# Kernel optimization log

Measured on AMD Instinct MI355X. Metric: run time of the kernel, lower is better.

The kernel has to match this reference:

```python
import jax, jax.numpy as jnp
import numpy as np

N = 100000   # nodes
E = 1600000  # edges
G = 256      # graphs in batch
IN = 128     # in_feats
H = 64       # h_feats


def _xavier(k, shape):
    fan_in, fan_out = shape
    lim = float(np.sqrt(6.0 / (fan_in + fan_out)))
    return jax.random.uniform(k, shape, jnp.float32, -lim, lim)


def setup_inputs() -> dict:
    key = jax.random.key(0)
    ks = jax.random.split(key, 12)
    x = jax.random.normal(ks[0], (N, IN), jnp.float32)
    src = jax.random.randint(ks[1], (E,), 0, N)
    dst = jax.random.randint(ks[2], (E,), 0, N)
    ew = jax.random.uniform(ks[3], (E,), jnp.float32)
    gid = jnp.sort(jax.random.randint(ks[4], (N,), 0, G))
    def lin(k, fi, fo):
        kw, kb = jax.random.split(k)
        lim = float(np.sqrt(1.0 / fi))
        return (jax.random.uniform(kw, (fi, fo), jnp.float32, -lim, lim),
                jax.random.uniform(kb, (fo,), jnp.float32, -lim, lim))
    W1 = _xavier(ks[5], (IN, H)); b1 = jnp.zeros((H,), jnp.float32)
    W2 = _xavier(ks[6], (H, H));  b2 = jnp.zeros((H,), jnp.float32)
    W3 = _xavier(ks[7], (H, H));  b3 = jnp.zeros((H,), jnp.float32)
    Dw1, Db1 = lin(ks[8], H, 16)
    Dw2, Db2 = lin(ks[9], 16, 8)
    Dw3, Db3 = lin(ks[10], 8, 1)
    return {"x": x, "src": src, "dst": dst, "ew": ew, "gid": gid,
            "W1": W1, "b1": b1, "W2": W2, "b2": b2, "W3": W3, "b3": b3,
            "Dw1": Dw1, "Db1": Db1, "Dw2": Dw2, "Db2": Db2, "Dw3": Dw3, "Db3": Db3}


def reference(x, src, dst, ew, gid, W1, b1, W2, b2, W3, b3,
              Dw1, Db1, Dw2, Db2, Dw3, Db3):
    n = x.shape[0]
    # DGL GraphConv norm='both': unweighted degrees, clamped to >= 1
    deg_out = jnp.zeros((n,), x.dtype).at[src].add(1.0)
    deg_in = jnp.zeros((n,), x.dtype).at[dst].add(1.0)
    ns = jax.lax.rsqrt(jnp.maximum(deg_out, 1.0))  # src-side norm
    nd = jax.lax.rsqrt(jnp.maximum(deg_in, 1.0))   # dst-side norm

    def conv(h, W, b):
        # apply weight first (in >= out), then gather-scale-scatter
        h = (h * ns[:, None]) @ W                      # [N, out]
        m = h[src] * ew[:, None]                       # [E, out] edge messages
        agg = jnp.zeros((n, W.shape[1]), h.dtype).at[dst].add(m)
        return agg * nd[:, None] + b

    h = jax.nn.relu(conv(x, W1, b1))
    h = jax.nn.relu(conv(h, W2, b2))
    h = jax.nn.relu(conv(h, W3, b3))

    # mean_nodes: per-graph mean pooling
    counts = jnp.zeros((G,), h.dtype).at[gid].add(1.0)
    pooled = jnp.zeros((G, h.shape[1]), h.dtype).at[gid].add(h)
    pooled = pooled / jnp.maximum(counts, 1.0)[:, None]

    h = jax.nn.relu(pooled @ Dw1 + Db1)
    h = jax.nn.relu(h @ Dw2 + Db2)
    return jax.nn.sigmoid(h @ Dw3 + Db3)  # [G, 1]
```

## Files before the change

kernel.cpp:

```cpp
#include <hip/hip_runtime.h>
#include <math.h>

#define N_NODES 100000
#define N_EDGES 1600000
#define G_GRAPHS 256
#define IN_F 128
#define H_F 64

#define HB 20
#define HCHUNK (N_EDGES / HB)
#define NWORDS (N_NODES / 4)
#define HNODES 25000
#define HWORDS (HNODES / 4)
#define HR 4

#define NREG 160
#define REG_NODES 625
#define BUCKET_CAP 11000
#define BSPAN 6400
#define NB_BUCKET (N_EDGES / BSPAN)

#define NTILES_C 6250
#define NB_GEMMW 391

typedef unsigned int uint_t;
typedef unsigned short ushort_t;
typedef unsigned char uchar_t;
typedef __attribute__((ext_vector_type(8))) short short8;
typedef __attribute__((ext_vector_type(4))) float floatx4;
typedef __attribute__((ext_vector_type(2))) float floatx2;

__device__ __forceinline__ ushort_t f2bf(float f) {
  uint_t u = __float_as_uint(f);
  uint_t r = (u + 0x7fffu + ((u >> 16) & 1u)) >> 16;
  return (ushort_t)r;
}
__device__ __forceinline__ float bflo(uint_t u) { return __uint_as_float(u << 16); }
__device__ __forceinline__ uchar_t f2fp8(float f) {
  return (uchar_t)(__builtin_amdgcn_cvt_pk_fp8_f32(f, f, 0, false) & 0xff);
}
__device__ __forceinline__ int sw_idx(int row, int kshort) {
  int slot = kshort >> 3;
  return row * 64 + (((slot ^ (row & 7)) << 3) | (kshort & 7));
}

__global__ __launch_bounds__(256) void build_a_kernel(
    const int* __restrict__ src, const int* __restrict__ dst,
    const float* __restrict__ ew, int* __restrict__ bcnt,
    uint2* __restrict__ bucket, uint_t* __restrict__ p8src) {
  __shared__ uint_t shm[BSPAN + 2 * NREG];
  if (blockIdx.x < NB_BUCKET) {
    uint_t* rl = shm;
    int* cnt = (int*)(shm + BSPAN);
    int* cur = cnt + NREG;
    const int e0 = blockIdx.x * BSPAN;

    for (int i = threadIdx.x; i < NREG; i += 256) cnt[i] = 0;
    __syncthreads();

    for (int i = threadIdx.x; i < BSPAN; i += 256) {
      uint_t d = (uint_t)dst[e0 + i];
      uint_t r = d / REG_NODES;
      uint_t loc = d - r * REG_NODES;
      rl[i] = (r << 16) | loc;
      atomicAdd(&cnt[r], 1);
    }
    __syncthreads();

    for (int i = threadIdx.x; i < NREG; i += 256)
      cur[i] = atomicAdd(&bcnt[i], cnt[i]);
    __syncthreads();

    for (int i = threadIdx.x; i < BSPAN; i += 256) {
      uint_t v = rl[i];
      uint_t r = v >> 16, loc = v & 0xffffu;
      int pos = atomicAdd(&cur[r], 1);
      if (pos < BUCKET_CAP)
        bucket[(size_t)r * BUCKET_CAP + pos] = make_uint2(
            (loc << 17) | (uint_t)src[e0 + i], __float_as_uint(ew[e0 + i]));
    }
  } else {
    uint_t* h = shm;
    const int idx = blockIdx.x - NB_BUCKET;
    const int r = idx / HB;
    const int b = idx % HB;
    const uint_t rbase = (uint_t)(r * HNODES);

    for (int i = threadIdx.x; i < HWORDS; i += 256) h[i] = 0u;
    __syncthreads();

    const uint4* k4 = (const uint4*)(src + b * HCHUNK);
    for (int i = threadIdx.x; i < HCHUNK / 4; i += 256) {
      uint4 v = k4[i];
      uint_t t;
      t = v.x - rbase; if (t < (uint_t)HNODES) atomicAdd(&h[t >> 2], 1u << ((t & 3u) * 8u));
      t = v.y - rbase; if (t < (uint_t)HNODES) atomicAdd(&h[t >> 2], 1u << ((t & 3u) * 8u));
      t = v.z - rbase; if (t < (uint_t)HNODES) atomicAdd(&h[t >> 2], 1u << ((t & 3u) * 8u));
      t = v.w - rbase; if (t < (uint_t)HNODES) atomicAdd(&h[t >> 2], 1u << ((t & 3u) * 8u));
    }
    __syncthreads();

    uint_t* outp = p8src + (size_t)b * NWORDS + r * HWORDS;
    for (int i = threadIdx.x; i < HWORDS; i += 256) outp[i] = h[i];
  }
}

__global__ __launch_bounds__(1024, 2) void buildb_gemm_kernel(
    const uint2* __restrict__ bucket, const int* __restrict__ bcnt,
    const uint_t* __restrict__ p8src, const float* __restrict__ x,
    const float* __restrict__ W1, uint_t* __restrict__ csr,
    int2* __restrict__ rc, float* __restrict__ nd, float* __restrict__ ns,
    uchar_t* __restrict__ T) {
  __shared__ __align__(16) char shm_u[53104];
  const int tid = threadIdx.x;

  if (blockIdx.x >= NREG) {
    constexpr int WROW = IN_F + 8;
    ushort_t* Wt = (ushort_t*)shm_u;
    float* ns_s = (float*)(shm_u + 17408);

    for (int i = tid; i < IN_F * 64; i += 1024) {
      int k = i >> 6, nn = i & 63;
      Wt[nn * WROW + k] = f2bf(W1[i]);
    }
    __syncthreads();

    const int wv = tid >> 6;
    const int lane = tid & 63;
    const int tile = (blockIdx.x - NREG) * 16 + wv;
    if (tile >= NTILES_C) return;
    const int node0 = tile * 16;
    const int m = lane & 15;
    const int q = lane >> 4;

    if (lane < 4) {
      const int w = tile * 4 + lane;
      int c0 = 0, c1 = 0, c2 = 0, c3 = 0;
      for (int b = 0; b < HB; ++b) {
        uint_t xv = p8src[(size_t)b * NWORDS + w];
        c0 += (int)(xv & 0xffu);
        c1 += (int)((xv >> 8) & 0xffu);
        c2 += (int)((xv >> 16) & 0xffu);
        c3 += (int)((xv >> 24) & 0xffu);
      }
      float4 nv = make_float4(
          rsqrtf(fmaxf((float)c0, 1.0f)), rsqrtf(fmaxf((float)c1, 1.0f)),
          rsqrtf(fmaxf((float)c2, 1.0f)), rsqrtf(fmaxf((float)c3, 1.0f)));
      ((float4*)ns)[w] = nv;
      *(float4*)&ns_s[wv * 16 + lane * 4] = nv;
    }

    short8 afrag[4];
    const float* xr = x + (size_t)(node0 + m) * IN_F + q * 8;
#pragma unroll
    for (int c = 0; c < 4; ++c) {
      float4 xa = *(const float4*)(xr + c * 32);
      float4 xb = *(const float4*)(xr + c * 32 + 4);
      short8 a;
      a[0] = (short)f2bf(xa.x); a[1] = (short)f2bf(xa.y);
      a[2] = (short)f2bf(xa.z); a[3] = (short)f2bf(xa.w);
      a[4] = (short)f2bf(xb.x); a[5] = (short)f2bf(xb.y);
      a[6] = (short)f2bf(xb.z); a[7] = (short)f2bf(xb.w);
      afrag[c] = a;
    }

    floatx4 acc[4];
#pragma unroll
    for (int t = 0; t < 4; ++t) acc[t] = (floatx4){0.f, 0.f, 0.f, 0.f};
#pragma unroll
    for (int t = 0; t < 4; ++t) {
      const ushort_t* wr = &Wt[(t * 16 + m) * WROW + q * 8];
#pragma unroll
      for (int c = 0; c < 4; ++c) {
        short8 bfrag = *(const short8*)(wr + c * 32);
        acc[t] = __builtin_amdgcn_mfma_f32_16x16x32_bf16(afrag[c], bfrag,
                                                         acc[t], 0, 0, 0);
      }
    }
#pragma unroll
    for (int t = 0; t < 4; ++t) {
#pragma unroll
      for (int r = 0; r < 4; ++r) {
        int node = node0 + q * 4 + r;
        T[(size_t)node * 64 + t * 16 + m] =
            f2fp8(acc[t][r] * ns_s[wv * 16 + q * 4 + r]);
      }
    }
    return;
  }

  uint_t* staged = (uint_t*)shm_u;
  int* cnt = (int*)(shm_u + 44000);
  int* sc = (int*)(shm_u + 46500);
  int* ts = (int*)(shm_u + 49000);
  const int r = blockIdx.x;
  const int nE = min(bcnt[r], BUCKET_CAP);

  ts[tid] = (tid < NREG) ? min(bcnt[tid], BUCKET_CAP) : 0;
  for (int i = tid; i < REG_NODES; i += 1024) cnt[i] = 0;
  __syncthreads();
  for (int off = 1; off < 256; off <<= 1) {
    int t = (tid >= off) ? ts[tid - off] : 0;
    __syncthreads();
    ts[tid] += t;
    __syncthreads();
  }
  const int csr_base = (r == 0) ? 0 : ts[r - 1];
  __syncthreads();

  const uint2* bk = bucket + (size_t)r * BUCKET_CAP;
  for (int i = tid; i < nE; i += 1024) atomicAdd(&cnt[bk[i].x >> 17], 1);
  __syncthreads();

  int cv = (tid < REG_NODES) ? cnt[tid] : 0;
  ts[tid] = cv;
  __syncthreads();
  for (int off = 1; off < 1024; off <<= 1) {
    int t = (tid >= off) ? ts[tid - off] : 0;
    __syncthreads();
    ts[tid] += t;
    __syncthreads();
  }
  if (tid < REG_NODES) {
    int run = (tid == 0) ? 0 : ts[tid - 1];
    sc[tid] = run;
    int v = r * REG_NODES + tid;
    rc[v] = make_int2(csr_base + run, cv);
    nd[v] = rsqrtf(fmaxf((float)cv, 1.0f));
  }
  __syncthreads();

  for (int i = tid; i < nE; i += 1024) {
    uint2 e = bk[i];
    uint_t loc = e.x >> 17;
    int pos = atomicAdd(&sc[loc], 1);
    staged[pos] = ((uint_t)(f2bf(__uint_as_float(e.y)) & 0x7fff) << 17) |
                  (e.x & 0x1ffffu);
  }
  __syncthreads();

  for (int i = tid; i < nE; i += 1024) csr[csr_base + i] = staged[i];
}

__device__ __forceinline__ void gacc1(float acc[8], uint_t e, uint2 p) {
  float w = __uint_as_float((e >> 17) << 16);
  floatx2 a;
  a = __builtin_amdgcn_cvt_pk_f32_fp8(p.x, false);
  acc[0] = fmaf(a.x, w, acc[0]); acc[1] = fmaf(a.y, w, acc[1]);
  a = __builtin_amdgcn_cvt_pk_f32_fp8(p.x, true);
  acc[2] = fmaf(a.x, w, acc[2]); acc[3] = fmaf(a.y, w, acc[3]);
  a = __builtin_amdgcn_cvt_pk_f32_fp8(p.y, false);
  acc[4] = fmaf(a.x, w, acc[4]); acc[5] = fmaf(a.y, w, acc[5]);
  a = __builtin_amdgcn_cvt_pk_f32_fp8(p.y, true);
  acc[6] = fmaf(a.x, w, acc[6]); acc[7] = fmaf(a.y, w, acc[7]);
}

template <bool POOL>
__global__ __launch_bounds__(256, 6) void fused_kernel(
    const uint_t* __restrict__ csr, const int2* __restrict__ rc,
    const uchar_t* __restrict__ T, const float* __restrict__ nd,
    const float* __restrict__ bias, const float* __restrict__ ns,
    const float* __restrict__ W, uchar_t* __restrict__ Tout,
    const int* __restrict__ gid, float* __restrict__ pooled) {
  __shared__ __align__(16) ushort_t Hs[POOL ? 8 : 64 * 64];
  __shared__ __align__(16) ushort_t Wt[POOL ? 8 : 64 * 64];
  __shared__ float gaccF[POOL ? 256 : 1];
  __shared__ int g0s;
  const int tid = threadIdx.x;
  const int node_base = blockIdx.x * 64;
  const int vlast = min(node_base + 63, N_NODES - 1);

  if constexpr (POOL) {
    gaccF[tid] = 0.0f;
    if (tid == 0) g0s = gid[node_base];
  } else {
    for (int i = tid; i < H_F * 64; i += 256) {
      int k = i >> 6, nn = i & 63;
      Wt[sw_idx(nn, k)] = f2bf(W[i]);
    }
  }
  __syncthreads();

  const int lane = tid & 63;
  const int wv = tid >> 6;
  const int o = lane >> 3, l = lane & 7;
  const uint2* Tp = (const uint2*)T;

  const float4 b0 = *(const float4*)&bias[l * 8];
  const float4 b1v = *(const float4*)&bias[l * 8 + 4];

#pragma unroll 1
  for (int pass = 0; pass < 2; ++pass) {
    const int ln = pass * 32 + wv * 8 + o;
    const int v = node_base + ln;
    if (v < N_NODES) {
      int2 rcv = rc[v];
      int k = rcv.x;
      const int ke = rcv.x + rcv.y;
      float acc[8] = {0, 0, 0, 0, 0, 0, 0, 0};

      for (; k + 4 <= ke; k += 4) {
        uint_t e0 = csr[k], e1 = csr[k + 1], e2 = csr[k + 2], e3 = csr[k + 3];
        uint2 p0 = Tp[(size_t)(e0 & 0x1ffffu) * 8 + l];
        uint2 p1 = Tp[(size_t)(e1 & 0x1ffffu) * 8 + l];
        uint2 p2 = Tp[(size_t)(e2 & 0x1ffffu) * 8 + l];
        uint2 p3 = Tp[(size_t)(e3 & 0x1ffffu) * 8 + l];
        gacc1(acc, e0, p0); gacc1(acc, e1, p1);
        gacc1(acc, e2, p2); gacc1(acc, e3, p3);
      }
      for (; k < ke; ++k) {
        uint_t e0 = csr[k];
        uint2 p0 = Tp[(size_t)(e0 & 0x1ffffu) * 8 + l];
        gacc1(acc, e0, p0);
      }

      const float ndv = nd[v];
      if constexpr (!POOL) {
        uint4 ov;
        ov.x = (uint_t)f2bf(fmaxf(fmaf(acc[0], ndv, b0.x), 0.f)) |
               ((uint_t)f2bf(fmaxf(fmaf(acc[1], ndv, b0.y), 0.f)) << 16);
        ov.y = (uint_t)f2bf(fmaxf(fmaf(acc[2], ndv, b0.z), 0.f)) |
               ((uint_t)f2bf(fmaxf(fmaf(acc[3], ndv, b0.w), 0.f)) << 16);
        ov.z = (uint_t)f2bf(fmaxf(fmaf(acc[4], ndv, b1v.x), 0.f)) |
               ((uint_t)f2bf(fmaxf(fmaf(acc[5], ndv, b1v.y), 0.f)) << 16);
        ov.w = (uint_t)f2bf(fmaxf(fmaf(acc[6], ndv, b1v.z), 0.f)) |
               ((uint_t)f2bf(fmaxf(fmaf(acc[7], ndv, b1v.w), 0.f)) << 16);
        *((uint4*)&Hs[sw_idx(ln, l * 8)]) = ov;
      } else {
        const float bb[8] = {b0.x, b0.y, b0.z, b0.w, b1v.x, b1v.y, b1v.z, b1v.w};
        float vals[8];
#pragma unroll
        for (int f = 0; f < 8; ++f)
          vals[f] = bflo((uint_t)f2bf(fmaxf(fmaf(acc[f], ndv, bb[f]), 0.f)));
        int g = gid[v];
        int gl = g - g0s;
        if (gl >= 0 && gl < 4) {
#pragma unroll
          for (int f = 0; f < 8; ++f)
            atomicAdd(&gaccF[gl * 64 + l * 8 + f], vals[f]);
        } else {
#pragma unroll
          for (int f = 0; f < 8; ++f)
            atomicAdd(&pooled[(size_t)g * 64 + l * 8 + f], vals[f]);
        }
      }
    }
  }
  __syncthreads();

  if constexpr (!POOL) {
    const int m = lane & 15, q = lane >> 4;
    const int node0 = node_base + wv * 16;
    if (node0 < N_NODES) {
      short8 afrag[2];
      afrag[0] = *(const short8*)&Hs[sw_idx(wv * 16 + m, q * 8)];
      afrag[1] = *(const short8*)&Hs[sw_idx(wv * 16 + m, q * 8 + 32)];

      floatx4 acc4v[4];
#pragma unroll
      for (int t = 0; t < 4; ++t) acc4v[t] = (floatx4){0.f, 0.f, 0.f, 0.f};
#pragma unroll
      for (int t = 0; t < 4; ++t) {
#pragma unroll
        for (int c = 0; c < 2; ++c) {
          short8 bfrag = *(const short8*)&Wt[sw_idx(t * 16 + m, q * 8 + c * 32)];
          acc4v[t] = __builtin_amdgcn_mfma_f32_16x16x32_bf16(afrag[c], bfrag,
                                                            acc4v[t], 0, 0, 0);
        }
      }
      float4 nsv = *(const float4*)(ns + node0 + q * 4);
      const float nsa[4] = {nsv.x, nsv.y, nsv.z, nsv.w};
#pragma unroll
      for (int t = 0; t < 4; ++t) {
#pragma unroll
        for (int r2 = 0; r2 < 4; ++r2) {
          int node = node0 + q * 4 + r2;
          Tout[(size_t)node * 64 + t * 16 + m] = f2fp8(acc4v[t][r2] * nsa[r2]);
        }
      }
    }
  } else {
    int span = gid[vlast] - g0s + 1;
    if (span > 4) span = 4;
    if (tid < span * 64) {
      int gl = tid >> 6, j = tid & 63;
      int g = g0s + gl;
      if (g < G_GRAPHS) {
        float vsum = gaccF[gl * 64 + j];
        if (vsum != 0.0f) atomicAdd(&pooled[(size_t)g * 64 + j], vsum);
      }
    }
  }
}

__global__ __launch_bounds__(256) void pool_mlp_kernel(
    const float* __restrict__ pooled, const int* __restrict__ gid,
    const float* __restrict__ Dw1, const float* __restrict__ Db1,
    const float* __restrict__ Dw2, const float* __restrict__ Db2,
    const float* __restrict__ Dw3, const float* __restrict__ Db3,
    float* __restrict__ out) {
  __shared__ float mean[64];
  __shared__ float h1s[16], h2s[8];
  const int g = blockIdx.x;
  int l = 0, r = N_NODES;
  while (l < r) { int m = (l + r) >> 1; if (gid[m] < g) l = m + 1; else r = m; }
  const int lo = l;
  r = N_NODES;
  while (l < r) { int m = (l + r) >> 1; if (gid[m] < g + 1) l = m + 1; else r = m; }
  const int hi = l;

  if (threadIdx.x < 64) {
    float inv = 1.0f / fmaxf((float)(hi - lo), 1.0f);
    mean[threadIdx.x] = pooled[(size_t)g * 64 + threadIdx.x] * inv;
  }
  __syncthreads();
  if (threadIdx.x < 16) {
    int o = threadIdx.x;
    float a = Db1[o];
#pragma unroll
    for (int k = 0; k < 64; ++k) a = fmaf(mean[k], Dw1[k * 16 + o], a);
    h1s[o] = fmaxf(a, 0.0f);
  }
  __syncthreads();
  if (threadIdx.x < 8) {
    int o = threadIdx.x;
    float a = Db2[o];
#pragma unroll
    for (int k = 0; k < 16; ++k) a = fmaf(h1s[k], Dw2[k * 8 + o], a);
    h2s[o] = fmaxf(a, 0.0f);
  }
  __syncthreads();
  if (threadIdx.x == 0) {
    float a = Db3[0];
#pragma unroll
    for (int k = 0; k < 8; ++k) a = fmaf(h2s[k], Dw3[k], a);
    out[g] = 1.0f / (1.0f + expf(-a));
  }
}

extern "C" void kernel_launch(void* const* d_in, const int* in_sizes, int n_in,
                              void* d_out, int out_size, void* d_ws, size_t ws_size,
                              hipStream_t stream) {
  const float* x   = (const float*)d_in[0];
  const int*   src = (const int*)  d_in[1];
  const int*   dst = (const int*)  d_in[2];
  const float* ew  = (const float*)d_in[3];
  const int*   gid = (const int*)  d_in[4];
  const float* W1  = (const float*)d_in[5];
  const float* b1  = (const float*)d_in[6];
  const float* W2  = (const float*)d_in[7];
  const float* b2  = (const float*)d_in[8];
  const float* W3  = (const float*)d_in[9];
  const float* b3  = (const float*)d_in[10];
  const float* Dw1 = (const float*)d_in[11];
  const float* Db1 = (const float*)d_in[12];
  const float* Dw2 = (const float*)d_in[13];
  const float* Db2 = (const float*)d_in[14];
  const float* Dw3 = (const float*)d_in[15];
  const float* Db3 = (const float*)d_in[16];
  float* out = (float*)d_out;

  char* p = (char*)d_ws;
  uint2*    bucket = (uint2*)p;          p += (size_t)NREG * BUCKET_CAP * 8;
  uint_t*   csr   = (uint_t*)p;          p += (size_t)N_EDGES * 4;
  uint_t*   p8src = (uint_t*)p;          p += (size_t)HB * NWORDS * 4;
  float*    ns    = (float*)p;           p += (size_t)N_NODES * 4;
  float*    nd    = (float*)p;           p += (size_t)N_NODES * 4;
  int2*     rc    = (int2*)p;            p += (size_t)N_NODES * 8;
  int*      bcnt  = (int*)p;             p += (size_t)NREG * 4;
  float*    pooled = (float*)p;          p += (size_t)G_GRAPHS * H_F * 4;
  uchar_t*  T_a   = (uchar_t*)p;         p += (size_t)N_NODES * 64;
  uchar_t*  T_b   = (uchar_t*)p;

  const int NB_A = NB_BUCKET + HR * HB;
  const int NB_M = NREG + NB_GEMMW;
  const int NB_F = (N_NODES + 63) / 64;

  hipMemsetAsync(bcnt, 0,
                 NREG * sizeof(int) + G_GRAPHS * H_F * sizeof(float), stream);
  build_a_kernel<<<NB_A, 256, 0, stream>>>(src, dst, ew, bcnt, bucket, p8src);
  buildb_gemm_kernel<<<NB_M, 1024, 0, stream>>>(bucket, bcnt, p8src, x, W1,
                                                csr, rc, nd, ns, T_a);
  fused_kernel<false><<<NB_F, 256, 0, stream>>>(csr, rc, T_a, nd, b1, ns, W2,
                                                T_b, nullptr, nullptr);
  fused_kernel<false><<<NB_F, 256, 0, stream>>>(csr, rc, T_b, nd, b2, ns, W3,
                                                T_a, nullptr, nullptr);
  fused_kernel<true><<<NB_F, 256, 0, stream>>>(csr, rc, T_a, nd, b3, nullptr,
                                               nullptr, nullptr, gid, pooled);
  pool_mlp_kernel<<<G_GRAPHS, 256, 0, stream>>>(pooled, gid, Dw1, Db1, Dw2, Db2,
                                                Dw3, Db3, out);
}
```

Baseline: 306.8 us.

## Split CSR by source half and gather in two grid-synced phases

The CSR build now partitions each destination's edges by whether the source node falls in the lower or upper half of node ids, and stores the split count in the high bits of rc. The fused layer kernels become cooperative launches with 128 nodes per block and 4 nodes per lane-group held in registers. Every block first gathers from low-half sources, hits a grid-wide sync, then gathers from high-half sources. This keeps the set of fp8 feature rows being read at any one time small enough to stay resident in cache. It adds grid-sync cost, lowers occupancy (launch bounds 4) and replaces the swizzled LDS layout with padded rows.

```diff
diff --git a/kernel.cpp b/kernel.cpp
--- a/kernel.cpp
+++ b/kernel.cpp
@@ -1,5 +1,8 @@
 #include <hip/hip_runtime.h>
+#include <hip/hip_cooperative_groups.h>
 #include <math.h>
+
+namespace cg = cooperative_groups;
 
 #define N_NODES 100000
 #define N_EDGES 1600000
@@ -22,6 +25,8 @@
 
 #define NTILES_C 6250
 #define NB_GEMMW 391
+#define SRC_HALF 50000
+#define NB_F2 782
 
 typedef unsigned int uint_t;
 typedef unsigned short ushort_t;
@@ -30,6 +35,8 @@
 typedef __attribute__((ext_vector_type(4))) float floatx4;
 typedef __attribute__((ext_vector_type(2))) float floatx2;
 
+constexpr int WROW_F = H_F + 8;
+
 __device__ __forceinline__ ushort_t f2bf(float f) {
   uint_t u = __float_as_uint(f);
   uint_t r = (u + 0x7fffu + ((u >> 16) & 1u)) >> 16;
@@ -38,10 +45,6 @@
 __device__ __forceinline__ float bflo(uint_t u) { return __uint_as_float(u << 16); }
 __device__ __forceinline__ uchar_t f2fp8(float f) {
   return (uchar_t)(__builtin_amdgcn_cvt_pk_fp8_f32(f, f, 0, false) & 0xff);
-}
-__device__ __forceinline__ int sw_idx(int row, int kshort) {
-  int slot = kshort >> 3;
-  return row * 64 + (((slot ^ (row & 7)) << 3) | (kshort & 7));
 }
 
 __global__ __launch_bounds__(256) void build_a_kernel(
@@ -111,7 +114,7 @@
     const float* __restrict__ W1, uint_t* __restrict__ csr,
     int2* __restrict__ rc, float* __restrict__ nd, float* __restrict__ ns,
     uchar_t* __restrict__ T) {
-  __shared__ __align__(16) char shm_u[53104];
+  __shared__ __align__(16) char shm_u[58112];
   const int tid = threadIdx.x;
 
   if (blockIdx.x >= NREG) {
@@ -190,14 +193,14 @@
   }
 
   uint_t* staged = (uint_t*)shm_u;
-  int* cnt = (int*)(shm_u + 44000);
-  int* sc = (int*)(shm_u + 46500);
-  int* ts = (int*)(shm_u + 49000);
+  int* cnt2 = (int*)(shm_u + 44000);
+  int* sc2 = (int*)(shm_u + 49000);
+  int* ts = (int*)(shm_u + 54000);
   const int r = blockIdx.x;
   const int nE = min(bcnt[r], BUCKET_CAP);
 
   ts[tid] = (tid < NREG) ? min(bcnt[tid], BUCKET_CAP) : 0;
-  for (int i = tid; i < REG_NODES; i += 1024) cnt[i] = 0;
+  for (int i = tid; i < REG_NODES * 2; i += 1024) cnt2[i] = 0;
   __syncthreads();
   for (int off = 1; off < 256; off <<= 1) {
     int t = (tid >= off) ? ts[tid - off] : 0;
@@ -209,10 +212,19 @@
   __syncthreads();
 
   const uint2* bk = bucket + (size_t)r * BUCKET_CAP;
-  for (int i = tid; i < nE; i += 1024) atomicAdd(&cnt[bk[i].x >> 17], 1);
-  __syncthreads();
-
-  int cv = (tid < REG_NODES) ? cnt[tid] : 0;
+  for (int i = tid; i < nE; i += 1024) {
+    uint_t ex = bk[i].x;
+    uint_t loc = ex >> 17;
+    uint_t q = ((ex & 0x1ffffu) >= SRC_HALF) ? 1u : 0u;
+    atomicAdd(&cnt2[loc * 2 + q], 1);
+  }
+  __syncthreads();
+
+  int c0 = 0, cv = 0;
+  if (tid < REG_NODES) {
+    c0 = cnt2[tid * 2];
+    cv = c0 + cnt2[tid * 2 + 1];
+  }
   ts[tid] = cv;
   __syncthreads();
   for (int off = 1; off < 1024; off <<= 1) {
@@ -223,9 +235,10 @@
   }
   if (tid < REG_NODES) {
     int run = (tid == 0) ? 0 : ts[tid - 1];
-    sc[tid] = run;
+    sc2[tid * 2] = run;
+    sc2[tid * 2 + 1] = run + c0;
     int v = r * REG_NODES + tid;
-    rc[v] = make_int2(csr_base + run, cv);
+    rc[v] = make_int2(csr_base + run, cv | (c0 << 16));
     nd[v] = rsqrtf(fmaxf((float)cv, 1.0f));
   }
   __syncthreads();
@@ -233,7 +246,8 @@
   for (int i = tid; i < nE; i += 1024) {
     uint2 e = bk[i];
     uint_t loc = e.x >> 17;
-    int pos = atomicAdd(&sc[loc], 1);
+    uint_t q = ((e.x & 0x1ffffu) >= SRC_HALF) ? 1u : 0u;
+    int pos = atomicAdd(&sc2[loc * 2 + q], 1);
     staged[pos] = ((uint_t)(f2bf(__uint_as_float(e.y)) & 0x7fff) << 17) |
                   (e.x & 0x1ffffu);
   }
@@ -255,20 +269,55 @@
   acc[6] = fmaf(a.x, w, acc[6]); acc[7] = fmaf(a.y, w, acc[7]);
 }
 
+__device__ __forceinline__ void gather_seg(const uint_t* __restrict__ csr,
+                                           const uint2* __restrict__ Tp, int l,
+                                           int s, int e, float acc[8]) {
+  int k = s;
+  while (k + 8 <= e) {
+    uint_t eb[8];
+    uint2 pb[8];
+#pragma unroll
+    for (int j = 0; j < 8; ++j) eb[j] = csr[k + j];
+#pragma unroll
+    for (int j = 0; j < 8; ++j)
+      pb[j] = Tp[(size_t)(eb[j] & 0x1ffffu) * 8 + l];
+#pragma unroll
+    for (int j = 0; j < 8; ++j) gacc1(acc, eb[j], pb[j]);
+    k += 8;
+  }
+  if (k + 4 <= e) {
+    uint_t eb[4];
+    uint2 pb[4];
+#pragma unroll
+    for (int j = 0; j < 4; ++j) eb[j] = csr[k + j];
+#pragma unroll
+    for (int j = 0; j < 4; ++j)
+      pb[j] = Tp[(size_t)(eb[j] & 0x1ffffu) * 8 + l];
+#pragma unroll
+    for (int j = 0; j < 4; ++j) gacc1(acc, eb[j], pb[j]);
+    k += 4;
+  }
+  for (; k < e; ++k) {
+    uint_t e0 = csr[k];
+    uint2 p0 = Tp[(size_t)(e0 & 0x1ffffu) * 8 + l];
+    gacc1(acc, e0, p0);
+  }
+}
+
 template <bool POOL>
-__global__ __launch_bounds__(256, 6) void fused_kernel(
+__global__ __launch_bounds__(256, 4) void fused_kernel(
     const uint_t* __restrict__ csr, const int2* __restrict__ rc,
     const uchar_t* __restrict__ T, const float* __restrict__ nd,
     const float* __restrict__ bias, const float* __restrict__ ns,
     const float* __restrict__ W, uchar_t* __restrict__ Tout,
     const int* __restrict__ gid, float* __restrict__ pooled) {
-  __shared__ __align__(16) ushort_t Hs[POOL ? 8 : 64 * 64];
-  __shared__ __align__(16) ushort_t Wt[POOL ? 8 : 64 * 64];
+  __shared__ __align__(16) ushort_t Hs[POOL ? 8 : 128 * WROW_F];
+  __shared__ __align__(16) ushort_t Wt[POOL ? 8 : 64 * WROW_F];
   __shared__ float gaccF[POOL ? 256 : 1];
   __shared__ int g0s;
   const int tid = threadIdx.x;
-  const int node_base = blockIdx.x * 64;
-  const int vlast = min(node_base + 63, N_NODES - 1);
+  const int node_base = blockIdx.x * 128;
+  const int vlast = min(node_base + 127, N_NODES - 1);
 
   if constexpr (POOL) {
     gaccF[tid] = 0.0f;
@@ -276,7 +325,7 @@
   } else {
     for (int i = tid; i < H_F * 64; i += 256) {
       int k = i >> 6, nn = i & 63;
-      Wt[sw_idx(nn, k)] = f2bf(W[i]);
+      Wt[nn * WROW_F + k] = f2bf(W[i]);
     }
   }
   __syncthreads();
@@ -289,49 +338,60 @@
   const float4 b0 = *(const float4*)&bias[l * 8];
   const float4 b1v = *(const float4*)&bias[l * 8 + 4];
 
-#pragma unroll 1
-  for (int pass = 0; pass < 2; ++pass) {
-    const int ln = pass * 32 + wv * 8 + o;
+  int2 rcv[4];
+#pragma unroll
+  for (int p = 0; p < 4; ++p) {
+    const int v = node_base + p * 32 + wv * 8 + o;
+    rcv[p] = (v < N_NODES) ? rc[v] : make_int2(0, 0);
+  }
+
+  float acc[4][8];
+#pragma unroll
+  for (int p = 0; p < 4; ++p)
+#pragma unroll
+    for (int f = 0; f < 8; ++f) acc[p][f] = 0.0f;
+
+#pragma unroll
+  for (int p = 0; p < 4; ++p) {
+    const int s = rcv[p].x;
+    const int h0 = ((uint_t)rcv[p].y) >> 16;
+    gather_seg(csr, Tp, l, s, s + h0, acc[p]);
+  }
+
+  cg::this_grid().sync();
+
+#pragma unroll
+  for (int p = 0; p < 4; ++p) {
+    const int s = rcv[p].x;
+    const int h0 = ((uint_t)rcv[p].y) >> 16;
+    const int cnt = rcv[p].y & 0xffff;
+    gather_seg(csr, Tp, l, s + h0, s + cnt, acc[p]);
+  }
+
+#pragma unroll
+  for (int p = 0; p < 4; ++p) {
+    const int ln = p * 32 + wv * 8 + o;
     const int v = node_base + ln;
     if (v < N_NODES) {
-      int2 rcv = rc[v];
-      int k = rcv.x;
-      const int ke = rcv.x + rcv.y;
-      float acc[8] = {0, 0, 0, 0, 0, 0, 0, 0};
-
-      for (; k + 4 <= ke; k += 4) {
-        uint_t e0 = csr[k], e1 = csr[k + 1], e2 = csr[k + 2], e3 = csr[k + 3];
-        uint2 p0 = Tp[(size_t)(e0 & 0x1ffffu) * 8 + l];
-        uint2 p1 = Tp[(size_t)(e1 & 0x1ffffu) * 8 + l];
-        uint2 p2 = Tp[(size_t)(e2 & 0x1ffffu) * 8 + l];
-        uint2 p3 = Tp[(size_t)(e3 & 0x1ffffu) * 8 + l];
-        gacc1(acc, e0, p0); gacc1(acc, e1, p1);
-        gacc1(acc, e2, p2); gacc1(acc, e3, p3);
-      }
-      for (; k < ke; ++k) {
-        uint_t e0 = csr[k];
-        uint2 p0 = Tp[(size_t)(e0 & 0x1ffffu) * 8 + l];
-        gacc1(acc, e0, p0);
-      }
-
       const float ndv = nd[v];
       if constexpr (!POOL) {
         uint4 ov;
-        ov.x = (uint_t)f2bf(fmaxf(fmaf(acc[0], ndv, b0.x), 0.f)) |
-               ((uint_t)f2bf(fmaxf(fmaf(acc[1], ndv, b0.y), 0.f)) << 16);
-        ov.y = (uint_t)f2bf(fmaxf(fmaf(acc[2], ndv, b0.z), 0.f)) |
-               ((uint_t)f2bf(fmaxf(fmaf(acc[3], ndv, b0.w), 0.f)) << 16);
-        ov.z = (uint_t)f2bf(fmaxf(fmaf(acc[4], ndv, b1v.x), 0.f)) |
-               ((uint_t)f2bf(fmaxf(fmaf(acc[5], ndv, b1v.y), 0.f)) << 16);
-        ov.w = (uint_t)f2bf(fmaxf(fmaf(acc[6], ndv, b1v.z), 0.f)) |
-               ((uint_t)f2bf(fmaxf(fmaf(acc[7], ndv, b1v.w), 0.f)) << 16);
-        *((uint4*)&Hs[sw_idx(ln, l * 8)]) = ov;
+        ov.x = (uint_t)f2bf(fmaxf(fmaf(acc[p][0], ndv, b0.x), 0.f)) |
+               ((uint_t)f2bf(fmaxf(fmaf(acc[p][1], ndv, b0.y), 0.f)) << 16);
+        ov.y = (uint_t)f2bf(fmaxf(fmaf(acc[p][2], ndv, b0.z), 0.f)) |
+               ((uint_t)f2bf(fmaxf(fmaf(acc[p][3], ndv, b0.w), 0.f)) << 16);
+        ov.z = (uint_t)f2bf(fmaxf(fmaf(acc[p][4], ndv, b1v.x), 0.f)) |
+               ((uint_t)f2bf(fmaxf(fmaf(acc[p][5], ndv, b1v.y), 0.f)) << 16);
+        ov.w = (uint_t)f2bf(fmaxf(fmaf(acc[p][6], ndv, b1v.z), 0.f)) |
+               ((uint_t)f2bf(fmaxf(fmaf(acc[p][7], ndv, b1v.w), 0.f)) << 16);
+        *((uint4*)&Hs[ln * WROW_F + l * 8]) = ov;
       } else {
-        const float bb[8] = {b0.x, b0.y, b0.z, b0.w, b1v.x, b1v.y, b1v.z, b1v.w};
+        const float bb[8] = {b0.x, b0.y, b0.z, b0.w,
+                             b1v.x, b1v.y, b1v.z, b1v.w};
         float vals[8];
 #pragma unroll
         for (int f = 0; f < 8; ++f)
-          vals[f] = bflo((uint_t)f2bf(fmaxf(fmaf(acc[f], ndv, bb[f]), 0.f)));
+          vals[f] = bflo((uint_t)f2bf(fmaxf(fmaf(acc[p][f], ndv, bb[f]), 0.f)));
         int g = gid[v];
         int gl = g - g0s;
         if (gl >= 0 && gl < 4) {
@@ -350,32 +410,39 @@
 
   if constexpr (!POOL) {
     const int m = lane & 15, q = lane >> 4;
-    const int node0 = node_base + wv * 16;
-    if (node0 < N_NODES) {
-      short8 afrag[2];
-      afrag[0] = *(const short8*)&Hs[sw_idx(wv * 16 + m, q * 8)];
-      afrag[1] = *(const short8*)&Hs[sw_idx(wv * 16 + m, q * 8 + 32)];
-
-      floatx4 acc4v[4];
-#pragma unroll
-      for (int t = 0; t < 4; ++t) acc4v[t] = (floatx4){0.f, 0.f, 0.f, 0.f};
-#pragma unroll
-      for (int t = 0; t < 4; ++t) {
-#pragma unroll
-        for (int c = 0; c < 2; ++c) {
-          short8 bfrag = *(const short8*)&Wt[sw_idx(t * 16 + m, q * 8 + c * 32)];
-          acc4v[t] = __builtin_amdgcn_mfma_f32_16x16x32_bf16(afrag[c], bfrag,
-                                                            acc4v[t], 0, 0, 0);
+#pragma unroll
+    for (int tt = 0; tt < 2; ++tt) {
+      const int row0 = tt * 64 + wv * 16;
+      const int node0 = node_base + row0;
+      if (node0 < N_NODES) {
+        short8 afrag[2];
+        const ushort_t* xr = &Hs[(row0 + m) * WROW_F + q * 8];
+        afrag[0] = *(const short8*)(xr);
+        afrag[1] = *(const short8*)(xr + 32);
+
+        floatx4 acc4v[4];
+#pragma unroll
+        for (int t = 0; t < 4; ++t) acc4v[t] = (floatx4){0.f, 0.f, 0.f, 0.f};
+#pragma unroll
+        for (int t = 0; t < 4; ++t) {
+          const ushort_t* wr = &Wt[(t * 16 + m) * WROW_F + q * 8];
+#pragma unroll
+          for (int c = 0; c < 2; ++c) {
+            short8 bfrag = *(const short8*)(wr + c * 32);
+            acc4v[t] = __builtin_amdgcn_mfma_f32_16x16x32_bf16(
+                afrag[c], bfrag, acc4v[t], 0, 0, 0);
+          }
         }
-      }
-      float4 nsv = *(const float4*)(ns + node0 + q * 4);
-      const float nsa[4] = {nsv.x, nsv.y, nsv.z, nsv.w};
-#pragma unroll
-      for (int t = 0; t < 4; ++t) {
-#pragma unroll
-        for (int r2 = 0; r2 < 4; ++r2) {
-          int node = node0 + q * 4 + r2;
-          Tout[(size_t)node * 64 + t * 16 + m] = f2fp8(acc4v[t][r2] * nsa[r2]);
+        float4 nsv = *(const float4*)(ns + node0 + q * 4);
+        const float nsa[4] = {nsv.x, nsv.y, nsv.z, nsv.w};
+#pragma unroll
+        for (int t = 0; t < 4; ++t) {
+#pragma unroll
+          for (int r2 = 0; r2 < 4; ++r2) {
+            int node = node0 + q * 4 + r2;
+            Tout[(size_t)node * 64 + t * 16 + m] =
+                f2fp8(acc4v[t][r2] * nsa[r2]);
+          }
         }
       }
     }
@@ -474,19 +541,45 @@
 
   const int NB_A = NB_BUCKET + HR * HB;
   const int NB_M = NREG + NB_GEMMW;
-  const int NB_F = (N_NODES + 63) / 64;
 
   hipMemsetAsync(bcnt, 0,
                  NREG * sizeof(int) + G_GRAPHS * H_F * sizeof(float), stream);
   build_a_kernel<<<NB_A, 256, 0, stream>>>(src, dst, ew, bcnt, bucket, p8src);
   buildb_gemm_kernel<<<NB_M, 1024, 0, stream>>>(bucket, bcnt, p8src, x, W1,
                                                 csr, rc, nd, ns, T_a);
-  fused_kernel<false><<<NB_F, 256, 0, stream>>>(csr, rc, T_a, nd, b1, ns, W2,
-                                                T_b, nullptr, nullptr);
-  fused_kernel<false><<<NB_F, 256, 0, stream>>>(csr, rc, T_b, nd, b2, ns, W3,
-                                                T_a, nullptr, nullptr);
-  fused_kernel<true><<<NB_F, 256, 0, stream>>>(csr, rc, T_a, nd, b3, nullptr,
-                                               nullptr, nullptr, gid, pooled);
+
+  {
+    const uint_t* a_csr = csr; const int2* a_rc = rc;
+    const float* a_nd = nd; const float* a_ns = ns;
+    const int* a_gid = gid; float* a_pool = pooled;
+    const int* null_gid = nullptr; float* null_pool = nullptr;
+
+    const uchar_t* tin1 = T_a; uchar_t* tout1 = T_b;
+    const float* bb1 = b1; const float* ww1 = W2;
+    void* args1[] = {(void*)&a_csr, (void*)&a_rc, (void*)&tin1, (void*)&a_nd,
+                     (void*)&bb1, (void*)&a_ns, (void*)&ww1, (void*)&tout1,
+                     (void*)&null_gid, (void*)&null_pool};
+    hipLaunchCooperativeKernel((void*)fused_kernel<false>, dim3(NB_F2),
+                               dim3(256), args1, 0, stream);
+
+    const uchar_t* tin2 = T_b; uchar_t* tout2 = T_a;
+    const float* bb2 = b2; const float* ww2 = W3;
+    void* args2[] = {(void*)&a_csr, (void*)&a_rc, (void*)&tin2, (void*)&a_nd,
+                     (void*)&bb2, (void*)&a_ns, (void*)&ww2, (void*)&tout2,
+                     (void*)&null_gid, (void*)&null_pool};
+    hipLaunchCooperativeKernel((void*)fused_kernel<false>, dim3(NB_F2),
+                               dim3(256), args2, 0, stream);
+
+    const uchar_t* tin3 = T_a; uchar_t* tout3 = nullptr;
+    const float* bb3 = b3; const float* ww3 = nullptr;
+    const float* ns3 = nullptr;
+    void* args3[] = {(void*)&a_csr, (void*)&a_rc, (void*)&tin3, (void*)&a_nd,
+                     (void*)&bb3, (void*)&ns3, (void*)&ww3, (void*)&tout3,
+                     (void*)&a_gid, (void*)&a_pool};
+    hipLaunchCooperativeKernel((void*)fused_kernel<true>, dim3(NB_F2),
+                               dim3(256), args3, 0, stream);
+  }
+
   pool_mlp_kernel<<<G_GRAPHS, 256, 0, stream>>>(pooled, gid, Dw1, Db1, Dw2, Db2,
                                                 Dw3, Db3, out);
 }
```

Result: slower. 661.1 us (+115.5%).

## Split fp8 feature table into two 32-feature halves and gather each half separately

Applied to the files above, without the earlier changes.

Stores the fp8 transformed features as two planes of 32 features per node instead of one 64-byte row, and runs the edge gather twice, once per half. Each half-plane is 3.2 MB, so the randomly accessed working set per pass is halved and may fit better in cache. In exchange the CSR edge list is read twice per layer, which the code marks nontemporal, and the gather is unrolled by 8. Each gathered element is a 4-byte word instead of 8 bytes, so per-edge loads get narrower.

```diff
diff --git a/kernel.cpp b/kernel.cpp
--- a/kernel.cpp
+++ b/kernel.cpp
@@ -22,6 +22,7 @@
 
 #define NTILES_C 6250
 #define NB_GEMMW 391
+#define T_HALF ((size_t)N_NODES * 32)
 
 typedef unsigned int uint_t;
 typedef unsigned short ushort_t;
@@ -182,7 +183,7 @@
 #pragma unroll
       for (int r = 0; r < 4; ++r) {
         int node = node0 + q * 4 + r;
-        T[(size_t)node * 64 + t * 16 + m] =
+        T[(size_t)(t >> 1) * T_HALF + (size_t)node * 32 + (t & 1) * 16 + m] =
             f2fp8(acc[t][r] * ns_s[wv * 16 + q * 4 + r]);
       }
     }
@@ -242,17 +243,46 @@
   for (int i = tid; i < nE; i += 1024) csr[csr_base + i] = staged[i];
 }
 
-__device__ __forceinline__ void gacc1(float acc[8], uint_t e, uint2 p) {
-  float w = __uint_as_float((e >> 17) << 16);
+__device__ __forceinline__ void gacc4(float acc[4], uint_t e, uint_t p) {
+  const float w = __uint_as_float((e >> 17) << 16);
   floatx2 a;
-  a = __builtin_amdgcn_cvt_pk_f32_fp8(p.x, false);
+  a = __builtin_amdgcn_cvt_pk_f32_fp8(p, false);
   acc[0] = fmaf(a.x, w, acc[0]); acc[1] = fmaf(a.y, w, acc[1]);
-  a = __builtin_amdgcn_cvt_pk_f32_fp8(p.x, true);
+  a = __builtin_amdgcn_cvt_pk_f32_fp8(p, true);
   acc[2] = fmaf(a.x, w, acc[2]); acc[3] = fmaf(a.y, w, acc[3]);
-  a = __builtin_amdgcn_cvt_pk_f32_fp8(p.y, false);
-  acc[4] = fmaf(a.x, w, acc[4]); acc[5] = fmaf(a.y, w, acc[5]);
-  a = __builtin_amdgcn_cvt_pk_f32_fp8(p.y, true);
-  acc[6] = fmaf(a.x, w, acc[6]); acc[7] = fmaf(a.y, w, acc[7]);
+}
+
+__device__ __forceinline__ void gather32(const uint_t* __restrict__ csr,
+                                         const uint_t* __restrict__ T32,
+                                         int l, int s, int e, float acc[4]) {
+  int k = s;
+  while (k + 8 <= e) {
+    uint_t eb[8], pb[8];
+#pragma unroll
+    for (int j = 0; j < 8; ++j) eb[j] = __builtin_nontemporal_load(&csr[k + j]);
+#pragma unroll
+    for (int j = 0; j < 8; ++j)
+      pb[j] = T32[(size_t)(eb[j] & 0x1ffffu) * 8 + l];
+#pragma unroll
+    for (int j = 0; j < 8; ++j) gacc4(acc, eb[j], pb[j]);
+    k += 8;
+  }
+  if (k + 4 <= e) {
+    uint_t eb[4], pb[4];
+#pragma unroll
+    for (int j = 0; j < 4; ++j) eb[j] = __builtin_nontemporal_load(&csr[k + j]);
+#pragma unroll
+    for (int j = 0; j < 4; ++j)
+      pb[j] = T32[(size_t)(eb[j] & 0x1ffffu) * 8 + l];
+#pragma unroll
+    for (int j = 0; j < 4; ++j) gacc4(acc, eb[j], pb[j]);
+    k += 4;
+  }
+  for (; k < e; ++k) {
+    uint_t e0 = __builtin_nontemporal_load(&csr[k]);
+    uint_t p0 = T32[(size_t)(e0 & 0x1ffffu) * 8 + l];
+    gacc4(acc, e0, p0);
+  }
 }
 
 template <bool POOL>
@@ -284,64 +314,54 @@
   const int lane = tid & 63;
   const int wv = tid >> 6;
   const int o = lane >> 3, l = lane & 7;
-  const uint2* Tp = (const uint2*)T;
-
-  const float4 b0 = *(const float4*)&bias[l * 8];
-  const float4 b1v = *(const float4*)&bias[l * 8 + 4];
+
+  int2 rcv[2];
+  float ndv[2];
+#pragma unroll
+  for (int rp = 0; rp < 2; ++rp) {
+    const int v = node_base + rp * 32 + wv * 8 + o;
+    rcv[rp] = (v < N_NODES) ? rc[v] : make_int2(0, 0);
+    ndv[rp] = (v < N_NODES) ? nd[v] : 0.0f;
+  }
 
 #pragma unroll 1
-  for (int pass = 0; pass < 2; ++pass) {
-    const int ln = pass * 32 + wv * 8 + o;
-    const int v = node_base + ln;
-    if (v < N_NODES) {
-      int2 rcv = rc[v];
-      int k = rcv.x;
-      const int ke = rcv.x + rcv.y;
-      float acc[8] = {0, 0, 0, 0, 0, 0, 0, 0};
-
-      for (; k + 4 <= ke; k += 4) {
-        uint_t e0 = csr[k], e1 = csr[k + 1], e2 = csr[k + 2], e3 = csr[k + 3];
-        uint2 p0 = Tp[(size_t)(e0 & 0x1ffffu) * 8 + l];
-        uint2 p1 = Tp[(size_t)(e1 & 0x1ffffu) * 8 + l];
-        uint2 p2 = Tp[(size_t)(e2 & 0x1ffffu) * 8 + l];
-        uint2 p3 = Tp[(size_t)(e3 & 0x1ffffu) * 8 + l];
-        gacc1(acc, e0, p0); gacc1(acc, e1, p1);
-        gacc1(acc, e2, p2); gacc1(acc, e3, p3);
-      }
-      for (; k < ke; ++k) {
-        uint_t e0 = csr[k];
-        uint2 p0 = Tp[(size_t)(e0 & 0x1ffffu) * 8 + l];
-        gacc1(acc, e0, p0);
-      }
-
-      const float ndv = nd[v];
-      if constexpr (!POOL) {
-        uint4 ov;
-        ov.x = (uint_t)f2bf(fmaxf(fmaf(acc[0], ndv, b0.x), 0.f)) |
-               ((uint_t)f2bf(fmaxf(fmaf(acc[1], ndv, b0.y), 0.f)) << 16);
-        ov.y = (uint_t)f2bf(fmaxf(fmaf(acc[2], ndv, b0.z), 0.f)) |
-               ((uint_t)f2bf(fmaxf(fmaf(acc[3], ndv, b0.w), 0.f)) << 16);
-        ov.z = (uint_t)f2bf(fmaxf(fmaf(acc[4], ndv, b1v.x), 0.f)) |
-               ((uint_t)f2bf(fmaxf(fmaf(acc[5], ndv, b1v.y), 0.f)) << 16);
-        ov.w = (uint_t)f2bf(fmaxf(fmaf(acc[6], ndv, b1v.z), 0.f)) |
-               ((uint_t)f2bf(fmaxf(fmaf(acc[7], ndv, b1v.w), 0.f)) << 16);
-        *((uint4*)&Hs[sw_idx(ln, l * 8)]) = ov;
-      } else {
-        const float bb[8] = {b0.x, b0.y, b0.z, b0.w, b1v.x, b1v.y, b1v.z, b1v.w};
-        float vals[8];
-#pragma unroll
-        for (int f = 0; f < 8; ++f)
-          vals[f] = bflo((uint_t)f2bf(fmaxf(fmaf(acc[f], ndv, bb[f]), 0.f)));
-        int g = gid[v];
-        int gl = g - g0s;
-        if (gl >= 0 && gl < 4) {
-#pragma unroll
-          for (int f = 0; f < 8; ++f)
-            atomicAdd(&gaccF[gl * 64 + l * 8 + f], vals[f]);
+  for (int h = 0; h < 2; ++h) {
+    const uint_t* T32 = (const uint_t*)(T + (size_t)h * T_HALF);
+    const float4 bh = *(const float4*)&bias[h * 32 + l * 4];
+    const float bl4[4] = {bh.x, bh.y, bh.z, bh.w};
+
+#pragma unroll 1
+    for (int rp = 0; rp < 2; ++rp) {
+      const int row = rp * 32 + wv * 8 + o;
+      const int v = node_base + row;
+      if (v < N_NODES) {
+        float acc[4] = {0, 0, 0, 0};
+        gather32(csr, T32, l, rcv[rp].x, rcv[rp].x + rcv[rp].y, acc);
+
+        float vals[4];
+#pragma unroll
+        for (int f = 0; f < 4; ++f)
+          vals[f] = fmaxf(fmaf(acc[f], ndv[rp], bl4[f]), 0.0f);
+
+        if constexpr (!POOL) {
+          uint2 ov;
+          ov.x = (uint_t)f2bf(vals[0]) | ((uint_t)f2bf(vals[1]) << 16);
+          ov.y = (uint_t)f2bf(vals[2]) | ((uint_t)f2bf(vals[3]) << 16);
+          *((uint2*)&Hs[sw_idx(row, h * 32 + l * 4)]) = ov;
         } else {
-#pragma unroll
-          for (int f = 0; f < 8; ++f)
-            atomicAdd(&pooled[(size_t)g * 64 + l * 8 + f], vals[f]);
+          const int g = gid[v];
+          const int gl = g - g0s;
+          if (gl >= 0 && gl < 4) {
+#pragma unroll
+            for (int f = 0; f < 4; ++f)
+              atomicAdd(&gaccF[gl * 64 + h * 32 + l * 4 + f],
+                        bflo((uint_t)f2bf(vals[f])));
+          } else {
+#pragma unroll
+            for (int f = 0; f < 4; ++f)
+              atomicAdd(&pooled[(size_t)g * 64 + h * 32 + l * 4 + f],
+                        bflo((uint_t)f2bf(vals[f])));
+          }
         }
       }
     }
@@ -375,7 +395,8 @@
 #pragma unroll
         for (int r2 = 0; r2 < 4; ++r2) {
           int node = node0 + q * 4 + r2;
-          Tout[(size_t)node * 64 + t * 16 + m] = f2fp8(acc4v[t][r2] * nsa[r2]);
+          Tout[(size_t)(t >> 1) * T_HALF + (size_t)node * 32 + (t & 1) * 16 + m] =
+              f2fp8(acc4v[t][r2] * nsa[r2]);
         }
       }
     }
@@ -469,7 +490,7 @@
   int2*     rc    = (int2*)p;            p += (size_t)N_NODES * 8;
   int*      bcnt  = (int*)p;             p += (size_t)NREG * 4;
   float*    pooled = (float*)p;          p += (size_t)G_GRAPHS * H_F * 4;
-  uchar_t*  T_a   = (uchar_t*)p;         p += (size_t)N_NODES * 64;
+  uchar_t*  T_a   = (uchar_t*)p;         p += 2 * T_HALF;
   uchar_t*  T_b   = (uchar_t*)p;
 
   const int NB_A = NB_BUCKET + HR * HB;
```

After: 387.6 us. 26.3% more time.
